# Optimization experiments

Measured on AMD Instinct MI355X. Metric: run time of the kernel, lower is better.

## Reference

```python
import jax, jax.numpy as jnp
import numpy as np

N_NODES = 50000
N_EDGES = 800000
IN_FEATS = 32
OUT_FEATS = 32
NUM_HEADS = 4


def setup_inputs() -> dict:
    key = jax.random.key(0)
    ks = jax.random.split(key, 12)
    H, F, IN = NUM_HEADS, OUT_FEATS, IN_FEATS
    h = jax.random.normal(ks[0], (N_NODES, IN), dtype=jnp.float32)
    src = jax.random.randint(ks[1], (N_EDGES,), 0, N_NODES, dtype=jnp.int64)
    dst = jax.random.randint(ks[2], (N_EDGES,), 0, N_NODES, dtype=jnp.int64)
    s = 0.1
    W_gat = jax.random.normal(ks[3], (IN, H * F), dtype=jnp.float32) * s
    attn_l = jax.random.normal(ks[4], (H, F), dtype=jnp.float32) * s
    attn_r = jax.random.normal(ks[5], (H, F), dtype=jnp.float32) * s
    W_ih = jax.random.normal(ks[6], (3 * F, H * F), dtype=jnp.float32) * s
    W_hh = jax.random.normal(ks[7], (3 * F, F), dtype=jnp.float32) * s
    b_ih = jax.random.normal(ks[8], (3 * F,), dtype=jnp.float32) * s
    b_hh = jax.random.normal(ks[9], (3 * F,), dtype=jnp.float32) * s
    return {"h": h, "W_gat": W_gat, "attn_l": attn_l, "attn_r": attn_r,
            "W_ih": W_ih, "W_hh": W_hh, "b_ih": b_ih, "b_hh": b_hh,
            "src": src, "dst": dst}


def reference(h, W_gat, attn_l, attn_r, W_ih, W_hh, b_ih, b_hh, src, dst):
    N = h.shape[0]
    H, F = attn_l.shape
    # --- GATConv ---
    feat = (h @ W_gat).reshape(N, H, F)                      # (N,H,F)
    el = jnp.einsum('nhf,hf->nh', feat, attn_l)              # (N,H)
    er = jnp.einsum('nhf,hf->nh', feat, attn_r)              # (N,H)
    e = jax.nn.leaky_relu(el[src] + er[dst], 0.2)            # (E,H) edge logits
    emax = jax.ops.segment_max(e, dst, num_segments=N)       # per-dst max (stable)
    ee = jnp.exp(e - emax[dst])
    denom = jax.ops.segment_sum(ee, dst, num_segments=N)
    alpha = ee / denom[dst]                                  # segment softmax (E,H)
    msg = feat[src] * alpha[:, :, None]                      # (E,H,F)
    agg = jax.ops.segment_sum(msg, dst, num_segments=N)      # (N,H,F)
    x = agg.reshape(N, H * F)
    # --- GRUCell (torch semantics, gate order r,z,n) ---
    gi = x @ W_ih.T + b_ih                                   # (N,3F)
    gh = h @ W_hh.T + b_hh                                   # (N,3F)
    i_r, i_z, i_n = jnp.split(gi, 3, axis=1)
    h_r, h_z, h_n = jnp.split(gh, 3, axis=1)
    r = jax.nn.sigmoid(i_r + h_r)
    z = jax.nn.sigmoid(i_z + h_z)
    n = jnp.tanh(i_n + r * h_n)
    h_new = (1.0 - z) * n + z * h
    return jax.nn.elu(h_new)
```

## Files before the change

### kernel.cpp

```cpp
#include <hip/hip_runtime.h>
#include <hip/hip_bf16.h>
#include <cmath>

#define N_NODES 50000
#define N_EDGES 800000
#define CAP 64

#define NBINS 196
#define BIN_CAP 8192
#define CUR_PAD 32

#define WCB_ITEMS (144 * 32)
#define WC_ITEMS (192 * 160)
#define PREP_ITEMS (WCB_ITEMS + WC_ITEMS)
#define PREP_BLOCKS ((PREP_ITEMS + 1023) / 1024)

#define P1_EPT 2
#define P1_EPB (1024 * P1_EPT)
#define P1_BLOCKS ((N_EDGES + P1_EPB - 1) / P1_EPB)
#define FEAT_BLOCKS ((N_NODES / 16 + 3) / 4)
#define AGGR_BLOCKS (N_NODES / 16)

typedef __attribute__((ext_vector_type(8))) short bf16x8;
typedef __attribute__((ext_vector_type(4))) float f32x4;

__device__ inline short bfbits(float x) {
    __hip_bfloat16 t = __float2bfloat16(x);
    return *reinterpret_cast<short*>(&t);
}

__device__ inline unsigned char f32_to_fp8(float x) {
    return (unsigned char)(__builtin_amdgcn_cvt_pk_fp8_f32(x, x, 0, false) & 0xff);
}

__global__ __launch_bounds__(1024) void k_part_prep(
        const int* __restrict__ src, const int* __restrict__ dst,
        int* __restrict__ bin_cursor, unsigned* __restrict__ bin_buf,
        const float* __restrict__ Wg, const float* __restrict__ al,
        const float* __restrict__ ar, const float* __restrict__ Wih,
        const float* __restrict__ Whh, __hip_bfloat16* __restrict__ Wcomb,
        __hip_bfloat16* __restrict__ Wc) {
    const int t = threadIdx.x;
    if (blockIdx.x >= P1_BLOCKS) {
        const int idx = (blockIdx.x - P1_BLOCKS) * 1024 + t;
        if (idx < WCB_ITEMS) {
            const int row = idx >> 5, k = idx & 31;
            float v = 0.f;
            if (row < 128) {
                v = Wg[k * 128 + row];
            } else if (row < 136) {
                const int hd = (row - 128) & 3;
                const float* a = (row < 132) ? (al + hd * 32) : (ar + hd * 32);
                const float* w = Wg + k * 128 + hd * 32;
#pragma unroll
                for (int f = 0; f < 32; ++f) v = fmaf(w[f], a[f], v);
            }
            Wcomb[idx] = __float2bfloat16(v);
        } else if (idx < PREP_ITEMS) {
            const int j = idx - WCB_ITEMS;
            const int r = j / 160, k = j - r * 160;
            float v = 0.f;
            if (r < 96) { if (k < 128) v = Wih[r * 128 + k]; }
            else        { if (k >= 128) v = Whh[(r - 96) * 32 + (k - 128)]; }
            Wc[j] = __float2bfloat16(v);
        }
        return;
    }
    __shared__ int bcnt[256], bofs[256], cur[256], gbase[256];
    __shared__ int wt4[4];
    __shared__ unsigned stage[P1_EPB];
    if (t < 256) bcnt[t] = 0;
    __syncthreads();
    int bn0 = -1, bn1 = -1;
    unsigned pk0 = 0, pk1 = 0;
    const int ebase = blockIdx.x * P1_EPB + t * 2;
    if (ebase < N_EDGES) {
        const int2 dd = *(const int2*)(dst + ebase);
        const int2 ss = *(const int2*)(src + ebase);
        bn0 = dd.x >> 8; pk0 = (unsigned)ss.x | ((unsigned)(dd.x & 255) << 16);
        bn1 = dd.y >> 8; pk1 = (unsigned)ss.y | ((unsigned)(dd.y & 255) << 16);
        atomicAdd(&bcnt[bn0], 1);
        atomicAdd(&bcnt[bn1], 1);
    }
    __syncthreads();
    int x = 0, vv = 0;
    if (t < 256) {
        vv = bcnt[t];
        x = vv;
        const int lane = t & 63;
#pragma unroll
        for (int m = 1; m < 64; m <<= 1) {
            const int y = __shfl_up(x, m, 64);
            if (lane >= m) x += y;
        }
        if (lane == 63) wt4[t >> 6] = x;
    }
    __syncthreads();
    if (t < 256) {
        const int wave4 = t >> 6;
        int wb = 0;
#pragma unroll
        for (int i = 0; i < 4; ++i) if (i < wave4) wb += wt4[i];
        const int off = wb + x - vv;
        bofs[t] = off;
        cur[t] = off;
        gbase[t] = (vv > 0) ? atomicAdd(&bin_cursor[t * CUR_PAD], vv) : 0;
    }
    __syncthreads();
    if (bn0 >= 0) {
        stage[atomicAdd(&cur[bn0], 1)] = pk0;
        stage[atomicAdd(&cur[bn1], 1)] = pk1;
    }
    __syncthreads();
    if (t < NBINS) {
        const int c = bcnt[t], o = bofs[t], g = gbase[t];
        unsigned* bb = bin_buf + (size_t)t * BIN_CAP;
        for (int j = 0; j < c; ++j) {
            const int gi = g + j;
            if (gi < BIN_CAP) bb[gi] = stage[o + j];
        }
    }
}

__global__ __launch_bounds__(256) void k_feat(
        const float* __restrict__ h, const __hip_bfloat16* __restrict__ Wcomb,
        unsigned char* __restrict__ feat, float* __restrict__ el,
        float* __restrict__ er) {
    __shared__ unsigned char sbuf8[4][16][136];
    const int t = threadIdx.x;
    const int lane = t & 63, wave = t >> 6;
    const int li = lane & 15, quad = lane >> 4;
    const int mt = blockIdx.x * 4 + wave;
    if (mt >= N_NODES / 16) return;
    const int m_base = mt * 16;
    bf16x8 a;
    {
        const float4* hp = (const float4*)(h + (size_t)(m_base + li) * 32 + quad * 8);
        const float4 f0 = hp[0], f1 = hp[1];
        a[0] = bfbits(f0.x); a[1] = bfbits(f0.y); a[2] = bfbits(f0.z); a[3] = bfbits(f0.w);
        a[4] = bfbits(f1.x); a[5] = bfbits(f1.y); a[6] = bfbits(f1.z); a[7] = bfbits(f1.w);
    }
    f32x4 acc[9];
#pragma unroll
    for (int j = 0; j < 9; ++j) acc[j] = (f32x4){0.f, 0.f, 0.f, 0.f};
#pragma unroll
    for (int j = 0; j < 9; ++j) {
        const bf16x8 b = *(const bf16x8*)(Wcomb + (size_t)(j * 16 + li) * 32 + quad * 8);
        acc[j] = __builtin_amdgcn_mfma_f32_16x16x32_bf16(a, b, acc[j], 0, 0, 0);
    }
#pragma unroll
    for (int j = 0; j < 8; ++j)
#pragma unroll
        for (int i = 0; i < 4; ++i)
            sbuf8[wave][quad * 4 + i][j * 16 + li] = f32_to_fp8(acc[j][i]);
    __builtin_amdgcn_wave_barrier();
#pragma unroll
    for (int rep = 0; rep < 4; ++rep) {
        const int row = rep * 4 + quad;
        const unsigned long long v = *(const unsigned long long*)(&sbuf8[wave][row][li * 8]);
        *(unsigned long long*)(feat + (size_t)(m_base + row) * 128 + li * 8) = v;
    }
    if (li < 8) {
#pragma unroll
        for (int i = 0; i < 4; ++i) {
            const int m = m_base + quad * 4 + i;
            if (li < 4) el[m * 4 + li] = acc[8][i];
            else        er[m * 4 + (li - 4)] = acc[8][i];
        }
    }
}

__global__ __launch_bounds__(256) void k_aggr_gru(
        const int* __restrict__ bin_cursor, const unsigned* __restrict__ bin_buf,
        const unsigned char* __restrict__ feat,
        const float* __restrict__ el, const float* __restrict__ er,
        const float* __restrict__ h, const __hip_bfloat16* __restrict__ Wc,
        const float* __restrict__ bih, const float* __restrict__ bhh,
        float* __restrict__ out) {
    __shared__ unsigned short list[16][CAP];
    __shared__ int lcnt[16];
    __shared__ __hip_bfloat16 xh_tile[16][160];
    __shared__ float eel_s[4][256];
    __shared__ float ex[2][3][16][16];
    const int t = threadIdx.x;
    const int wave = t >> 6;
    const int lane = t & 63;
    const int pb = blockIdx.x >> 4, six = blockIdx.x & 15;
    const int mbase = blockIdx.x * 16;

    if (t < 16) lcnt[t] = 0;
    __syncthreads();

    const int cbn = min(bin_cursor[pb * CUR_PAD], BIN_CAP);
    const uint4* bb4 = (const uint4*)(bin_buf + (size_t)pb * BIN_CAP);
    for (int i = t * 4; i < cbn; i += 1024) {
        const uint4 p4 = bb4[i >> 2];
#pragma unroll
        for (int k = 0; k < 4; ++k) {
            if (i + k < cbn) {
                const unsigned p = (&p4.x)[k];
                const int local = (p >> 16) & 255;
                if ((local >> 4) == six) {
                    const int dl = local & 15;
                    const int pos = atomicAdd(&lcnt[dl], 1);
                    if (pos < CAP) list[dl][pos] = (unsigned short)(p & 0xffff);
                }
            }
        }
    }
    __syncthreads();

    float* eel = eel_s[wave];
    const int hs = lane & 3;
    const int eh = lane >> 5;
    const int fl = lane & 31;
    const int hq = fl >> 3;
    for (int u = 0; u < 4; ++u) {
        const int row = wave * 4 + u;
        const int n = mbase + row;
        const float ern = er[n * 4 + hs];
        const int cnt = min(lcnt[row], CAP);
        const unsigned short* sl = list[row];
        float a0 = 0.f, a1 = 0.f, a2 = 0.f, a3 = 0.f, psum = 0.f;
#pragma unroll
        for (int p = 0; p < 4; ++p) {
            const int j = p * 64 + lane;
            if (j < cnt * 4) {
                const int s = sl[j >> 2];
                float v = el[s * 4 + hs] + ern;
                v = v > 0.f ? v : 0.2f * v;
                const float e = __expf(v);
                eel[j] = e;
                psum += e;
            }
        }
        __builtin_amdgcn_wave_barrier();
        int i = 0;
        for (; i + 8 <= cnt; i += 8) {
            const int s0 = sl[i + eh],     s1 = sl[i + 2 + eh];
            const int s2 = sl[i + 4 + eh], s3 = sl[i + 6 + eh];
            const unsigned u0 = *(const unsigned*)(feat + (size_t)s0 * 128 + fl * 4);
            const unsigned u1 = *(const unsigned*)(feat + (size_t)s1 * 128 + fl * 4);
            const unsigned u2 = *(const unsigned*)(feat + (size_t)s2 * 128 + fl * 4);
            const unsigned u3 = *(const unsigned*)(feat + (size_t)s3 * 128 + fl * 4);
            const float w0 = eel[(i + eh) * 4 + hq];
            const float w1 = eel[(i + 2 + eh) * 4 + hq];
            const float w2 = eel[(i + 4 + eh) * 4 + hq];
            const float w3 = eel[(i + 6 + eh) * 4 + hq];
            a0 = fmaf(w0, __builtin_amdgcn_cvt_f32_fp8(u0, 0), a0);
            a1 = fmaf(w0, __builtin_amdgcn_cvt_f32_fp8(u0, 1), a1);
            a2 = fmaf(w0, __builtin_amdgcn_cvt_f32_fp8(u0, 2), a2);
            a3 = fmaf(w0, __builtin_amdgcn_cvt_f32_fp8(u0, 3), a3);
            a0 = fmaf(w1, __builtin_amdgcn_cvt_f32_fp8(u1, 0), a0);
            a1 = fmaf(w1, __builtin_amdgcn_cvt_f32_fp8(u1, 1), a1);
            a2 = fmaf(w1, __builtin_amdgcn_cvt_f32_fp8(u1, 2), a2);
            a3 = fmaf(w1, __builtin_amdgcn_cvt_f32_fp8(u1, 3), a3);
            a0 = fmaf(w2, __builtin_amdgcn_cvt_f32_fp8(u2, 0), a0);
            a1 = fmaf(w2, __builtin_amdgcn_cvt_f32_fp8(u2, 1), a1);
            a2 = fmaf(w2, __builtin_amdgcn_cvt_f32_fp8(u2, 2), a2);
            a3 = fmaf(w2, __builtin_amdgcn_cvt_f32_fp8(u2, 3), a3);
            a0 = fmaf(w3, __builtin_amdgcn_cvt_f32_fp8(u3, 0), a0);
            a1 = fmaf(w3, __builtin_amdgcn_cvt_f32_fp8(u3, 1), a1);
            a2 = fmaf(w3, __builtin_amdgcn_cvt_f32_fp8(u3, 2), a2);
            a3 = fmaf(w3, __builtin_amdgcn_cvt_f32_fp8(u3, 3), a3);
        }
        for (; i < cnt; i += 2) {
            const int e2 = i + eh;
            if (e2 < cnt) {
                const int s0 = sl[e2];
                const unsigned u0 = *(const unsigned*)(feat + (size_t)s0 * 128 + fl * 4);
                const float w0 = eel[e2 * 4 + hq];
                a0 = fmaf(w0, __builtin_amdgcn_cvt_f32_fp8(u0, 0), a0);
                a1 = fmaf(w0, __builtin_amdgcn_cvt_f32_fp8(u0, 1), a1);
                a2 = fmaf(w0, __builtin_amdgcn_cvt_f32_fp8(u0, 2), a2);
                a3 = fmaf(w0, __builtin_amdgcn_cvt_f32_fp8(u0, 3), a3);
            }
        }
        __builtin_amdgcn_wave_barrier();
        a0 += __shfl_xor(a0, 32, 64);
        a1 += __shfl_xor(a1, 32, 64);
        a2 += __shfl_xor(a2, 32, 64);
        a3 += __shfl_xor(a3, 32, 64);
#pragma unroll
        for (int m = 4; m < 64; m <<= 1) psum += __shfl_xor(psum, m, 64);
        const float dn = __shfl(psum, hq, 64);
        const float inv = (cnt > 0) ? 1.f / dn : 0.f;
        if (lane < 32) {
            __hip_bfloat162 p0, p1;
            p0.x = __float2bfloat16(a0 * inv); p0.y = __float2bfloat16(a1 * inv);
            p1.x = __float2bfloat16(a2 * inv); p1.y = __float2bfloat16(a3 * inv);
            __hip_bfloat162* xp = (__hip_bfloat162*)&xh_tile[row][0];
            xp[lane * 2]     = p0;
            xp[lane * 2 + 1] = p1;
            xh_tile[row][128 + lane] = __float2bfloat16(h[(size_t)n * 32 + lane]);
        }
    }
    __syncthreads();

    const int li = lane & 15, quad = lane >> 4;
    const int cb = wave >> 1;
    const int ghrole = wave & 1;
    bf16x8 a[5];
#pragma unroll
    for (int s = 0; s < 5; ++s)
        a[s] = *(const bf16x8*)((const char*)&xh_tile[0][0] + li * 320 + s * 64 + quad * 16);
    f32x4 acc[3];
#pragma unroll
    for (int g = 0; g < 3; ++g) {
        acc[g] = (f32x4){0.f, 0.f, 0.f, 0.f};
        const int j = g * 2 + cb + ghrole * 6;
        const bf16x8* bp = (const bf16x8*)(Wc + (size_t)(j * 16 + li) * 160 + quad * 8);
        acc[g] = __builtin_amdgcn_mfma_f32_16x16x32_bf16(a[0], bp[0],  acc[g], 0, 0, 0);
        acc[g] = __builtin_amdgcn_mfma_f32_16x16x32_bf16(a[1], bp[4],  acc[g], 0, 0, 0);
        acc[g] = __builtin_amdgcn_mfma_f32_16x16x32_bf16(a[2], bp[8],  acc[g], 0, 0, 0);
        acc[g] = __builtin_amdgcn_mfma_f32_16x16x32_bf16(a[3], bp[12], acc[g], 0, 0, 0);
        acc[g] = __builtin_amdgcn_mfma_f32_16x16x32_bf16(a[4], bp[16], acc[g], 0, 0, 0);
    }
    if (ghrole) {
#pragma unroll
        for (int g = 0; g < 3; ++g)
#pragma unroll
            for (int i = 0; i < 4; ++i)
                ex[cb][g][quad * 4 + i][li] = acc[g][i];
    }
    __syncthreads();
    if (!ghrole) {
        const int c = cb * 16 + li;
        const float bir = bih[c],      bhr = bhh[c];
        const float biz = bih[32 + c], bhz = bhh[32 + c];
        const float bin = bih[64 + c], bhn = bhh[64 + c];
#pragma unroll
        for (int i = 0; i < 4; ++i) {
            const int row = quad * 4 + i;
            const int m = mbase + row;
            const float gr = acc[0][i] + bir + ex[cb][0][row][li] + bhr;
            const float gz = acc[1][i] + biz + ex[cb][1][row][li] + bhz;
            const float r = 1.f / (1.f + expf(-gr));
            const float z = 1.f / (1.f + expf(-gz));
            const float nn = tanhf(acc[2][i] + bin + r * (ex[cb][2][row][li] + bhn));
            const float hv = h[(size_t)m * 32 + c];
            const float hn = (1.f - z) * nn + z * hv;
            out[(size_t)m * 32 + c] = hn > 0.f ? hn : expm1f(hn);
        }
    }
}

extern "C" void kernel_launch(void* const* d_in, const int* in_sizes, int n_in,
                              void* d_out, int out_size, void* d_ws, size_t ws_size,
                              hipStream_t stream) {
    const float* h   = (const float*)d_in[0];
    const float* Wg  = (const float*)d_in[1];
    const float* al  = (const float*)d_in[2];
    const float* ar  = (const float*)d_in[3];
    const float* Wih = (const float*)d_in[4];
    const float* Whh = (const float*)d_in[5];
    const float* bih = (const float*)d_in[6];
    const float* bhh = (const float*)d_in[7];
    const int* src   = (const int*)d_in[8];
    const int* dst   = (const int*)d_in[9];
    float* out = (float*)d_out;

    float* el = (float*)d_ws;
    float* er = el + (size_t)N_NODES * 4;
    unsigned char* feat8 = (unsigned char*)(er + (size_t)N_NODES * 4);
    __hip_bfloat16* Wc    = (__hip_bfloat16*)(feat8 + (size_t)N_NODES * 128);
    __hip_bfloat16* Wcomb = Wc + WC_ITEMS;
    int* bin_cursor = (int*)(Wcomb + WCB_ITEMS);
    unsigned* bin_buf = (unsigned*)(bin_cursor + NBINS * CUR_PAD);

    hipMemsetAsync(bin_cursor, 0, NBINS * CUR_PAD * sizeof(int), stream);
    k_part_prep<<<P1_BLOCKS + PREP_BLOCKS, 1024, 0, stream>>>(
        src, dst, bin_cursor, bin_buf, Wg, al, ar, Wih, Whh, Wcomb, Wc);
    k_feat<<<FEAT_BLOCKS, 256, 0, stream>>>(h, Wcomb, feat8, el, er);
    k_aggr_gru<<<AGGR_BLOCKS, 256, 0, stream>>>(
        bin_cursor, bin_buf, feat8, el, er, h, Wc, bih, bhh, out);
}
```

Before: 155.6 us.

## Aggregate raw bf16 inputs per head, then apply W_gat after aggregation

Instead of projecting every node to 128-wide fp8 features and gathering those per edge, the kernel gathers the 32-wide bf16 copy of h per edge. It accumulates one weighted sum per head and applies W_gat once per destination node with MFMA after aggregation, using the linearity of the projection. The separate feature kernel is folded into the partition/prep launch, which now also converts h to bf16 and computes el/er. This cuts per-edge gather bytes and removes a launch, at the cost of four times more FMAs per gathered element and an extra small matmul in the aggregation kernel.

```diff
diff --git a/kernel.cpp b/kernel.cpp
--- a/kernel.cpp
+++ b/kernel.cpp
@@ -10,15 +10,19 @@
 #define BIN_CAP 8192
 #define CUR_PAD 32
 
-#define WCB_ITEMS (144 * 32)
-#define WC_ITEMS (192 * 160)
-#define PREP_ITEMS (WCB_ITEMS + WC_ITEMS)
-#define PREP_BLOCKS ((PREP_ITEMS + 1023) / 1024)
-
 #define P1_EPT 2
 #define P1_EPB (1024 * P1_EPT)
 #define P1_BLOCKS ((N_EDGES + P1_EPB - 1) / P1_EPB)
-#define FEAT_BLOCKS ((N_NODES / 16 + 3) / 4)
+
+#define HB_BLOCKS 98
+#define ELR_BLOCKS 196
+#define WC_BLOCKS 30
+#define NB_HB  (P1_BLOCKS)
+#define NB_ELR (NB_HB + HB_BLOCKS)
+#define NB_WC  (NB_ELR + ELR_BLOCKS)
+#define NB_WGB (NB_WC + WC_BLOCKS)
+#define PREP_TOTAL (NB_WGB + 1)
+
 #define AGGR_BLOCKS (N_NODES / 16)
 
 typedef __attribute__((ext_vector_type(8))) short bf16x8;
@@ -28,159 +32,177 @@
     __hip_bfloat16 t = __float2bfloat16(x);
     return *reinterpret_cast<short*>(&t);
 }
-
-__device__ inline unsigned char f32_to_fp8(float x) {
-    return (unsigned char)(__builtin_amdgcn_cvt_pk_fp8_f32(x, x, 0, false) & 0xff);
+__device__ inline unsigned short bfu16(float x) {
+    __hip_bfloat16 t = __float2bfloat16(x);
+    return *reinterpret_cast<unsigned short*>(&t);
 }
 
 __global__ __launch_bounds__(1024) void k_part_prep(
         const int* __restrict__ src, const int* __restrict__ dst,
         int* __restrict__ bin_cursor, unsigned* __restrict__ bin_buf,
-        const float* __restrict__ Wg, const float* __restrict__ al,
-        const float* __restrict__ ar, const float* __restrict__ Wih,
-        const float* __restrict__ Whh, __hip_bfloat16* __restrict__ Wcomb,
-        __hip_bfloat16* __restrict__ Wc) {
+        const float* __restrict__ h, const float* __restrict__ Wg,
+        const float* __restrict__ al, const float* __restrict__ ar,
+        const float* __restrict__ Wih, const float* __restrict__ Whh,
+        unsigned short* __restrict__ hb, float* __restrict__ el,
+        float* __restrict__ er, __hip_bfloat16* __restrict__ Wc,
+        __hip_bfloat16* __restrict__ Wgb) {
     const int t = threadIdx.x;
-    if (blockIdx.x >= P1_BLOCKS) {
-        const int idx = (blockIdx.x - P1_BLOCKS) * 1024 + t;
-        if (idx < WCB_ITEMS) {
-            const int row = idx >> 5, k = idx & 31;
+    __shared__ union {
+        struct {
+            int bcnt[256], bofs[256], cur[256], gbase[256];
+            int wt4[4];
+            unsigned stage[P1_EPB];
+        } part;
+        __hip_bfloat16 vlr[16][32];
+    } sm;
+
+    if (blockIdx.x < P1_BLOCKS) {
+        int* bcnt = sm.part.bcnt; int* bofs = sm.part.bofs;
+        int* cur = sm.part.cur;   int* gbase = sm.part.gbase;
+        int* wt4 = sm.part.wt4;   unsigned* stage = sm.part.stage;
+        if (t < 256) bcnt[t] = 0;
+        __syncthreads();
+        int bn0 = -1, bn1 = -1;
+        unsigned pk0 = 0, pk1 = 0;
+        const int ebase = blockIdx.x * P1_EPB + t * 2;
+        if (ebase < N_EDGES) {
+            const int2 dd = *(const int2*)(dst + ebase);
+            const int2 ss = *(const int2*)(src + ebase);
+            bn0 = dd.x >> 8; pk0 = (unsigned)ss.x | ((unsigned)(dd.x & 255) << 16);
+            bn1 = dd.y >> 8; pk1 = (unsigned)ss.y | ((unsigned)(dd.y & 255) << 16);
+            atomicAdd(&bcnt[bn0], 1);
+            atomicAdd(&bcnt[bn1], 1);
+        }
+        __syncthreads();
+        int x = 0, vv = 0;
+        if (t < 256) {
+            vv = bcnt[t];
+            x = vv;
+            const int lane = t & 63;
+#pragma unroll
+            for (int m = 1; m < 64; m <<= 1) {
+                const int y = __shfl_up(x, m, 64);
+                if (lane >= m) x += y;
+            }
+            if (lane == 63) wt4[t >> 6] = x;
+        }
+        __syncthreads();
+        if (t < 256) {
+            const int wave4 = t >> 6;
+            int wb = 0;
+#pragma unroll
+            for (int i = 0; i < 4; ++i) if (i < wave4) wb += wt4[i];
+            const int off = wb + x - vv;
+            bofs[t] = off;
+            cur[t] = off;
+            gbase[t] = (vv > 0) ? atomicAdd(&bin_cursor[t * CUR_PAD], vv) : 0;
+        }
+        __syncthreads();
+        if (bn0 >= 0) {
+            stage[atomicAdd(&cur[bn0], 1)] = pk0;
+            stage[atomicAdd(&cur[bn1], 1)] = pk1;
+        }
+        __syncthreads();
+        if (t < NBINS) {
+            const int c = bcnt[t], o = bofs[t], g = gbase[t];
+            unsigned* bb = bin_buf + (size_t)t * BIN_CAP;
+            for (int j = 0; j < c; ++j) {
+                const int gi = g + j;
+                if (gi < BIN_CAP) bb[gi] = stage[o + j];
+            }
+        }
+        return;
+    }
+    if (blockIdx.x < NB_ELR) {
+        const int idx = (blockIdx.x - NB_HB) * 1024 + t;
+        const int base = idx * 16;
+        if (base < N_NODES * 32) {
+            const float4* hp = (const float4*)(h + base);
+            const float4 v0 = hp[0], v1 = hp[1], v2 = hp[2], v3 = hp[3];
+            unsigned o[8];
+            o[0] = (unsigned)bfu16(v0.x) | ((unsigned)bfu16(v0.y) << 16);
+            o[1] = (unsigned)bfu16(v0.z) | ((unsigned)bfu16(v0.w) << 16);
+            o[2] = (unsigned)bfu16(v1.x) | ((unsigned)bfu16(v1.y) << 16);
+            o[3] = (unsigned)bfu16(v1.z) | ((unsigned)bfu16(v1.w) << 16);
+            o[4] = (unsigned)bfu16(v2.x) | ((unsigned)bfu16(v2.y) << 16);
+            o[5] = (unsigned)bfu16(v2.z) | ((unsigned)bfu16(v2.w) << 16);
+            o[6] = (unsigned)bfu16(v3.x) | ((unsigned)bfu16(v3.y) << 16);
+            o[7] = (unsigned)bfu16(v3.z) | ((unsigned)bfu16(v3.w) << 16);
+            uint4* op = (uint4*)(hb + base);
+            op[0] = (uint4){o[0], o[1], o[2], o[3]};
+            op[1] = (uint4){o[4], o[5], o[6], o[7]};
+        }
+        return;
+    }
+    if (blockIdx.x < NB_WC) {
+        if (t < 512) {
+            const int col = t >> 5, k = t & 31;
             float v = 0.f;
-            if (row < 128) {
-                v = Wg[k * 128 + row];
-            } else if (row < 136) {
-                const int hd = (row - 128) & 3;
-                const float* a = (row < 132) ? (al + hd * 32) : (ar + hd * 32);
+            if (col < 8) {
+                const int hd = col & 3;
+                const float* a = (col < 4) ? (al + hd * 32) : (ar + hd * 32);
                 const float* w = Wg + k * 128 + hd * 32;
 #pragma unroll
                 for (int f = 0; f < 32; ++f) v = fmaf(w[f], a[f], v);
             }
-            Wcomb[idx] = __float2bfloat16(v);
-        } else if (idx < PREP_ITEMS) {
-            const int j = idx - WCB_ITEMS;
-            const int r = j / 160, k = j - r * 160;
-            float v = 0.f;
-            if (r < 96) { if (k < 128) v = Wih[r * 128 + k]; }
-            else        { if (k >= 128) v = Whh[(r - 96) * 32 + (k - 128)]; }
-            Wc[j] = __float2bfloat16(v);
+            sm.vlr[col][k] = __float2bfloat16(v);
+        }
+        __syncthreads();
+        const int wave = t >> 6, lane = t & 63;
+        const int li = lane & 15, quad = lane >> 4;
+        const int mt = (blockIdx.x - NB_ELR) * 16 + wave;
+        if (mt >= AGGR_BLOCKS) return;
+        const int m_base = mt * 16;
+        bf16x8 a;
+        {
+            const float4* hp = (const float4*)(h + (size_t)(m_base + li) * 32 + quad * 8);
+            const float4 f0 = hp[0], f1 = hp[1];
+            a[0] = bfbits(f0.x); a[1] = bfbits(f0.y); a[2] = bfbits(f0.z); a[3] = bfbits(f0.w);
+            a[4] = bfbits(f1.x); a[5] = bfbits(f1.y); a[6] = bfbits(f1.z); a[7] = bfbits(f1.w);
+        }
+        const bf16x8 b = *(const bf16x8*)(&sm.vlr[li][0] + quad * 8);
+        f32x4 acc = (f32x4){0.f, 0.f, 0.f, 0.f};
+        acc = __builtin_amdgcn_mfma_f32_16x16x32_bf16(a, b, acc, 0, 0, 0);
+        if (li < 8) {
+#pragma unroll
+            for (int i = 0; i < 4; ++i) {
+                const int m = m_base + quad * 4 + i;
+                if (li < 4) el[m * 4 + li] = acc[i];
+                else        er[m * 4 + (li - 4)] = acc[i];
+            }
         }
         return;
     }
-    __shared__ int bcnt[256], bofs[256], cur[256], gbase[256];
-    __shared__ int wt4[4];
-    __shared__ unsigned stage[P1_EPB];
-    if (t < 256) bcnt[t] = 0;
-    __syncthreads();
-    int bn0 = -1, bn1 = -1;
-    unsigned pk0 = 0, pk1 = 0;
-    const int ebase = blockIdx.x * P1_EPB + t * 2;
-    if (ebase < N_EDGES) {
-        const int2 dd = *(const int2*)(dst + ebase);
-        const int2 ss = *(const int2*)(src + ebase);
-        bn0 = dd.x >> 8; pk0 = (unsigned)ss.x | ((unsigned)(dd.x & 255) << 16);
-        bn1 = dd.y >> 8; pk1 = (unsigned)ss.y | ((unsigned)(dd.y & 255) << 16);
-        atomicAdd(&bcnt[bn0], 1);
-        atomicAdd(&bcnt[bn1], 1);
-    }
-    __syncthreads();
-    int x = 0, vv = 0;
-    if (t < 256) {
-        vv = bcnt[t];
-        x = vv;
-        const int lane = t & 63;
-#pragma unroll
-        for (int m = 1; m < 64; m <<= 1) {
-            const int y = __shfl_up(x, m, 64);
-            if (lane >= m) x += y;
-        }
-        if (lane == 63) wt4[t >> 6] = x;
-    }
-    __syncthreads();
-    if (t < 256) {
-        const int wave4 = t >> 6;
-        int wb = 0;
-#pragma unroll
-        for (int i = 0; i < 4; ++i) if (i < wave4) wb += wt4[i];
-        const int off = wb + x - vv;
-        bofs[t] = off;
-        cur[t] = off;
-        gbase[t] = (vv > 0) ? atomicAdd(&bin_cursor[t * CUR_PAD], vv) : 0;
-    }
-    __syncthreads();
-    if (bn0 >= 0) {
-        stage[atomicAdd(&cur[bn0], 1)] = pk0;
-        stage[atomicAdd(&cur[bn1], 1)] = pk1;
-    }
-    __syncthreads();
-    if (t < NBINS) {
-        const int c = bcnt[t], o = bofs[t], g = gbase[t];
-        unsigned* bb = bin_buf + (size_t)t * BIN_CAP;
-        for (int j = 0; j < c; ++j) {
-            const int gi = g + j;
-            if (gi < BIN_CAP) bb[gi] = stage[o + j];
-        }
-    }
-}
-
-__global__ __launch_bounds__(256) void k_feat(
-        const float* __restrict__ h, const __hip_bfloat16* __restrict__ Wcomb,
-        unsigned char* __restrict__ feat, float* __restrict__ el,
-        float* __restrict__ er) {
-    __shared__ unsigned char sbuf8[4][16][136];
-    const int t = threadIdx.x;
-    const int lane = t & 63, wave = t >> 6;
-    const int li = lane & 15, quad = lane >> 4;
-    const int mt = blockIdx.x * 4 + wave;
-    if (mt >= N_NODES / 16) return;
-    const int m_base = mt * 16;
-    bf16x8 a;
-    {
-        const float4* hp = (const float4*)(h + (size_t)(m_base + li) * 32 + quad * 8);
-        const float4 f0 = hp[0], f1 = hp[1];
-        a[0] = bfbits(f0.x); a[1] = bfbits(f0.y); a[2] = bfbits(f0.z); a[3] = bfbits(f0.w);
-        a[4] = bfbits(f1.x); a[5] = bfbits(f1.y); a[6] = bfbits(f1.z); a[7] = bfbits(f1.w);
-    }
-    f32x4 acc[9];
-#pragma unroll
-    for (int j = 0; j < 9; ++j) acc[j] = (f32x4){0.f, 0.f, 0.f, 0.f};
-#pragma unroll
-    for (int j = 0; j < 9; ++j) {
-        const bf16x8 b = *(const bf16x8*)(Wcomb + (size_t)(j * 16 + li) * 32 + quad * 8);
-        acc[j] = __builtin_amdgcn_mfma_f32_16x16x32_bf16(a, b, acc[j], 0, 0, 0);
-    }
-#pragma unroll
-    for (int j = 0; j < 8; ++j)
-#pragma unroll
-        for (int i = 0; i < 4; ++i)
-            sbuf8[wave][quad * 4 + i][j * 16 + li] = f32_to_fp8(acc[j][i]);
-    __builtin_amdgcn_wave_barrier();
-#pragma unroll
-    for (int rep = 0; rep < 4; ++rep) {
-        const int row = rep * 4 + quad;
-        const unsigned long long v = *(const unsigned long long*)(&sbuf8[wave][row][li * 8]);
-        *(unsigned long long*)(feat + (size_t)(m_base + row) * 128 + li * 8) = v;
-    }
-    if (li < 8) {
-#pragma unroll
-        for (int i = 0; i < 4; ++i) {
-            const int m = m_base + quad * 4 + i;
-            if (li < 4) el[m * 4 + li] = acc[8][i];
-            else        er[m * 4 + (li - 4)] = acc[8][i];
-        }
+    if (blockIdx.x < NB_WGB) {
+        const int idx = (blockIdx.x - NB_WC) * 1024 + t;
+        const int r = idx / 160, k = idx - r * 160;
+        float v = 0.f;
+        if (r < 96) { if (k < 128) v = Wih[r * 128 + k]; }
+        else        { if (k >= 128) v = Whh[(r - 96) * 32 + (k - 128)]; }
+        Wc[idx] = __float2bfloat16(v);
+        return;
+    }
+#pragma unroll
+    for (int jj = 0; jj < 4; ++jj) {
+        const int id = t * 4 + jj;
+        const int k = id & 31, f = (id >> 5) & 31, hd = id >> 10;
+        Wgb[id] = __float2bfloat16(Wg[k * 128 + hd * 32 + f]);
     }
 }
 
 __global__ __launch_bounds__(256) void k_aggr_gru(
         const int* __restrict__ bin_cursor, const unsigned* __restrict__ bin_buf,
-        const unsigned char* __restrict__ feat,
+        const unsigned char* __restrict__ hb,
         const float* __restrict__ el, const float* __restrict__ er,
         const float* __restrict__ h, const __hip_bfloat16* __restrict__ Wc,
+        const __hip_bfloat16* __restrict__ Wgb,
         const float* __restrict__ bih, const float* __restrict__ bhh,
         float* __restrict__ out) {
     __shared__ unsigned short list[16][CAP];
     __shared__ int lcnt[16];
     __shared__ __hip_bfloat16 xh_tile[16][160];
     __shared__ float eel_s[4][256];
+    __shared__ unsigned Sn[16][64];
     __shared__ float ex[2][3][16][16];
     const int t = threadIdx.x;
     const int wave = t >> 6;
@@ -212,16 +234,18 @@
 
     float* eel = eel_s[wave];
     const int hs = lane & 3;
-    const int eh = lane >> 5;
-    const int fl = lane & 31;
-    const int hq = fl >> 3;
+    const int eq = lane >> 4;
+    const int dw = lane & 15;
     for (int u = 0; u < 4; ++u) {
         const int row = wave * 4 + u;
         const int n = mbase + row;
         const float ern = er[n * 4 + hs];
         const int cnt = min(lcnt[row], CAP);
         const unsigned short* sl = list[row];
-        float a0 = 0.f, a1 = 0.f, a2 = 0.f, a3 = 0.f, psum = 0.f;
+        eel[lane] = 0.f; eel[64 + lane] = 0.f;
+        eel[128 + lane] = 0.f; eel[192 + lane] = 0.f;
+        __builtin_amdgcn_wave_barrier();
+        float psum = 0.f;
 #pragma unroll
         for (int p = 0; p < 4; ++p) {
             const int j = p * 64 + lane;
@@ -235,64 +259,75 @@
             }
         }
         __builtin_amdgcn_wave_barrier();
-        int i = 0;
-        for (; i + 8 <= cnt; i += 8) {
-            const int s0 = sl[i + eh],     s1 = sl[i + 2 + eh];
-            const int s2 = sl[i + 4 + eh], s3 = sl[i + 6 + eh];
-            const unsigned u0 = *(const unsigned*)(feat + (size_t)s0 * 128 + fl * 4);
-            const unsigned u1 = *(const unsigned*)(feat + (size_t)s1 * 128 + fl * 4);
-            const unsigned u2 = *(const unsigned*)(feat + (size_t)s2 * 128 + fl * 4);
-            const unsigned u3 = *(const unsigned*)(feat + (size_t)s3 * 128 + fl * 4);
-            const float w0 = eel[(i + eh) * 4 + hq];
-            const float w1 = eel[(i + 2 + eh) * 4 + hq];
-            const float w2 = eel[(i + 4 + eh) * 4 + hq];
-            const float w3 = eel[(i + 6 + eh) * 4 + hq];
-            a0 = fmaf(w0, __builtin_amdgcn_cvt_f32_fp8(u0, 0), a0);
-            a1 = fmaf(w0, __builtin_amdgcn_cvt_f32_fp8(u0, 1), a1);
-            a2 = fmaf(w0, __builtin_amdgcn_cvt_f32_fp8(u0, 2), a2);
-            a3 = fmaf(w0, __builtin_amdgcn_cvt_f32_fp8(u0, 3), a3);
-            a0 = fmaf(w1, __builtin_amdgcn_cvt_f32_fp8(u1, 0), a0);
-            a1 = fmaf(w1, __builtin_amdgcn_cvt_f32_fp8(u1, 1), a1);
-            a2 = fmaf(w1, __builtin_amdgcn_cvt_f32_fp8(u1, 2), a2);
-            a3 = fmaf(w1, __builtin_amdgcn_cvt_f32_fp8(u1, 3), a3);
-            a0 = fmaf(w2, __builtin_amdgcn_cvt_f32_fp8(u2, 0), a0);
-            a1 = fmaf(w2, __builtin_amdgcn_cvt_f32_fp8(u2, 1), a1);
-            a2 = fmaf(w2, __builtin_amdgcn_cvt_f32_fp8(u2, 2), a2);
-            a3 = fmaf(w2, __builtin_amdgcn_cvt_f32_fp8(u2, 3), a3);
-            a0 = fmaf(w3, __builtin_amdgcn_cvt_f32_fp8(u3, 0), a0);
-            a1 = fmaf(w3, __builtin_amdgcn_cvt_f32_fp8(u3, 1), a1);
-            a2 = fmaf(w3, __builtin_amdgcn_cvt_f32_fp8(u3, 2), a2);
-            a3 = fmaf(w3, __builtin_amdgcn_cvt_f32_fp8(u3, 3), a3);
-        }
-        for (; i < cnt; i += 2) {
-            const int e2 = i + eh;
-            if (e2 < cnt) {
-                const int s0 = sl[e2];
-                const unsigned u0 = *(const unsigned*)(feat + (size_t)s0 * 128 + fl * 4);
-                const float w0 = eel[e2 * 4 + hq];
-                a0 = fmaf(w0, __builtin_amdgcn_cvt_f32_fp8(u0, 0), a0);
-                a1 = fmaf(w0, __builtin_amdgcn_cvt_f32_fp8(u0, 1), a1);
-                a2 = fmaf(w0, __builtin_amdgcn_cvt_f32_fp8(u0, 2), a2);
-                a3 = fmaf(w0, __builtin_amdgcn_cvt_f32_fp8(u0, 3), a3);
+        float a00 = 0.f, a01 = 0.f, a10 = 0.f, a11 = 0.f;
+        float a20 = 0.f, a21 = 0.f, a30 = 0.f, a31 = 0.f;
+        for (int i = 0; i < cnt; i += 16) {
+            int e[4];
+#pragma unroll
+            for (int j = 0; j < 4; ++j) {
+                const int ee = i + j * 4 + eq;
+                e[j] = (ee < cnt) ? sl[ee] : 0;
+            }
+            unsigned q[4];
+#pragma unroll
+            for (int j = 0; j < 4; ++j)
+                q[j] = *(const unsigned*)(hb + (size_t)e[j] * 64 + dw * 4);
+#pragma unroll
+            for (int j = 0; j < 4; ++j) {
+                const int ee = i + j * 4 + eq;
+                const float lo = __uint_as_float(q[j] << 16);
+                const float hi = __uint_as_float(q[j] & 0xffff0000u);
+                const float w0 = eel[ee * 4 + 0];
+                const float w1 = eel[ee * 4 + 1];
+                const float w2 = eel[ee * 4 + 2];
+                const float w3 = eel[ee * 4 + 3];
+                a00 = fmaf(w0, lo, a00); a01 = fmaf(w0, hi, a01);
+                a10 = fmaf(w1, lo, a10); a11 = fmaf(w1, hi, a11);
+                a20 = fmaf(w2, lo, a20); a21 = fmaf(w2, hi, a21);
+                a30 = fmaf(w3, lo, a30); a31 = fmaf(w3, hi, a31);
             }
         }
         __builtin_amdgcn_wave_barrier();
-        a0 += __shfl_xor(a0, 32, 64);
-        a1 += __shfl_xor(a1, 32, 64);
-        a2 += __shfl_xor(a2, 32, 64);
-        a3 += __shfl_xor(a3, 32, 64);
+#pragma unroll
+        for (int m = 16; m < 64; m <<= 1) {
+            a00 += __shfl_xor(a00, m, 64); a01 += __shfl_xor(a01, m, 64);
+            a10 += __shfl_xor(a10, m, 64); a11 += __shfl_xor(a11, m, 64);
+            a20 += __shfl_xor(a20, m, 64); a21 += __shfl_xor(a21, m, 64);
+            a30 += __shfl_xor(a30, m, 64); a31 += __shfl_xor(a31, m, 64);
+        }
 #pragma unroll
         for (int m = 4; m < 64; m <<= 1) psum += __shfl_xor(psum, m, 64);
-        const float dn = __shfl(psum, hq, 64);
-        const float inv = (cnt > 0) ? 1.f / dn : 0.f;
-        if (lane < 32) {
-            __hip_bfloat162 p0, p1;
-            p0.x = __float2bfloat16(a0 * inv); p0.y = __float2bfloat16(a1 * inv);
-            p1.x = __float2bfloat16(a2 * inv); p1.y = __float2bfloat16(a3 * inv);
-            __hip_bfloat162* xp = (__hip_bfloat162*)&xh_tile[row][0];
-            xp[lane * 2]     = p0;
-            xp[lane * 2 + 1] = p1;
+        const float inv0 = (cnt > 0) ? 1.f / __shfl(psum, 0, 64) : 0.f;
+        const float inv1 = (cnt > 0) ? 1.f / __shfl(psum, 1, 64) : 0.f;
+        const float inv2 = (cnt > 0) ? 1.f / __shfl(psum, 2, 64) : 0.f;
+        const float inv3 = (cnt > 0) ? 1.f / __shfl(psum, 3, 64) : 0.f;
+        if (lane < 16) {
+            Sn[row][0 * 16 + lane] = (unsigned)bfu16(a00 * inv0) | ((unsigned)bfu16(a01 * inv0) << 16);
+            Sn[row][1 * 16 + lane] = (unsigned)bfu16(a10 * inv1) | ((unsigned)bfu16(a11 * inv1) << 16);
+            Sn[row][2 * 16 + lane] = (unsigned)bfu16(a20 * inv2) | ((unsigned)bfu16(a21 * inv2) << 16);
+            Sn[row][3 * 16 + lane] = (unsigned)bfu16(a30 * inv3) | ((unsigned)bfu16(a31 * inv3) << 16);
+        }
+        if (lane < 32)
             xh_tile[row][128 + lane] = __float2bfloat16(h[(size_t)n * 32 + lane]);
+    }
+    __syncthreads();
+
+    {
+        const int li = lane & 15, quad = lane >> 4;
+        const int head = wave;
+        const __hip_bfloat16* snb = (const __hip_bfloat16*)&Sn[0][0];
+        const bf16x8 aS = *(const bf16x8*)(snb + li * 128 + head * 32 + quad * 8);
+        const bf16x8 b0 = *(const bf16x8*)(Wgb + (size_t)(head * 32 + li) * 32 + quad * 8);
+        const bf16x8 b1 = *(const bf16x8*)(Wgb + (size_t)(head * 32 + 16 + li) * 32 + quad * 8);
+        f32x4 c0 = (f32x4){0.f, 0.f, 0.f, 0.f};
+        f32x4 c1 = (f32x4){0.f, 0.f, 0.f, 0.f};
+        c0 = __builtin_amdgcn_mfma_f32_16x16x32_bf16(aS, b0, c0, 0, 0, 0);
+        c1 = __builtin_amdgcn_mfma_f32_16x16x32_bf16(aS, b1, c1, 0, 0, 0);
+#pragma unroll
+        for (int i = 0; i < 4; ++i) {
+            const int row = quad * 4 + i;
+            xh_tile[row][head * 32 + li]      = __float2bfloat16(c0[i]);
+            xh_tile[row][head * 32 + 16 + li] = __float2bfloat16(c1[i]);
         }
     }
     __syncthreads();
@@ -360,18 +395,19 @@
     const int* dst   = (const int*)d_in[9];
     float* out = (float*)d_out;
 
-    float* el = (float*)d_ws;
+    unsigned short* hb = (unsigned short*)d_ws;
+    unsigned* bin_buf = (unsigned*)(hb + (size_t)N_NODES * 32);
+    float* el = (float*)(bin_buf + (size_t)NBINS * BIN_CAP);
     float* er = el + (size_t)N_NODES * 4;
-    unsigned char* feat8 = (unsigned char*)(er + (size_t)N_NODES * 4);
-    __hip_bfloat16* Wc    = (__hip_bfloat16*)(feat8 + (size_t)N_NODES * 128);
-    __hip_bfloat16* Wcomb = Wc + WC_ITEMS;
-    int* bin_cursor = (int*)(Wcomb + WCB_ITEMS);
-    unsigned* bin_buf = (unsigned*)(bin_cursor + NBINS * CUR_PAD);
+    __hip_bfloat16* Wc  = (__hip_bfloat16*)(er + (size_t)N_NODES * 4);
+    __hip_bfloat16* Wgb = Wc + 30720;
+    int* bin_cursor = (int*)(Wgb + 4096);
 
     hipMemsetAsync(bin_cursor, 0, NBINS * CUR_PAD * sizeof(int), stream);
-    k_part_prep<<<P1_BLOCKS + PREP_BLOCKS, 1024, 0, stream>>>(
-        src, dst, bin_cursor, bin_buf, Wg, al, ar, Wih, Whh, Wcomb, Wc);
-    k_feat<<<FEAT_BLOCKS, 256, 0, stream>>>(h, Wcomb, feat8, el, er);
+    k_part_prep<<<PREP_TOTAL, 1024, 0, stream>>>(
+        src, dst, bin_cursor, bin_buf, h, Wg, al, ar, Wih, Whh,
+        hb, el, er, Wc, Wgb);
     k_aggr_gru<<<AGGR_BLOCKS, 256, 0, stream>>>(
-        bin_cursor, bin_buf, feat8, el, er, h, Wc, bih, bhh, out);
+        bin_cursor, bin_buf, (const unsigned char*)hb, el, er, h, Wc, Wgb,
+        bih, bhh, out);
 }
```

New measurement: 150.0 us. 1.04x faster.
